# Kernel optimization log

Hardware: AMD Instinct MI355X
Metric: run time of the kernel (lower is better)

Reference implementation:

```python
import jax, jax.numpy as jnp
import numpy as np

DIM = 1024
HEADS = 16
DIM_HEAD = 64
INNER = HEADS * DIM_HEAD
SCALE = 8.0  # default scale in plain_cosine_sim_attention
EPS = 1e-5


def setup_inputs() -> dict:
    key = jax.random.key(0)
    ks = jax.random.split(key, 5)
    b, n = 2, 2048
    x = jax.random.normal(ks[0], (b, n, DIM), dtype=jnp.float32)
    ln_w = jnp.ones((DIM,), dtype=jnp.float32)
    ln_b = jnp.zeros((DIM,), dtype=jnp.float32)
    W_qkv = jax.random.normal(ks[1], (DIM, 3 * INNER), dtype=jnp.float32) * (DIM ** -0.5)
    W_out = jax.random.normal(ks[2], (INNER, DIM), dtype=jnp.float32) * (INNER ** -0.5)
    return {"x": x, "ln_w": ln_w, "ln_b": ln_b, "W_qkv": W_qkv, "W_out": W_out}


def _l2norm(t):
    return t / jnp.clip(jnp.linalg.norm(t, axis=-1, keepdims=True), 1e-12)


def reference(x, ln_w, ln_b, W_qkv, W_out):
    b, n, _ = x.shape
    # LayerNorm
    mu = jnp.mean(x, axis=-1, keepdims=True)
    var = jnp.var(x, axis=-1, keepdims=True)
    xn = (x - mu) * jax.lax.rsqrt(var + EPS) * ln_w + ln_b
    # QKV projection (no bias)
    qkv = xn @ W_qkv  # [b, n, 3*inner]
    q, k, v = jnp.split(qkv, 3, axis=-1)
    # [b, n, h*d] -> [b, h, n, d]
    def to_heads(t):
        return t.reshape(b, n, HEADS, DIM_HEAD).transpose(0, 2, 1, 3)
    q, k, v = to_heads(q), to_heads(k), to_heads(v)
    # cosine-sim attention: l2-normalize q, k then scaled dot product
    q = _l2norm(q)
    k = _l2norm(k)
    sim = jnp.einsum('bhid,bhjd->bhij', q, k) * SCALE
    # causal mask
    causal = jnp.tril(jnp.ones((n, n), dtype=bool))
    sim = jnp.where(causal, sim, jnp.finfo(sim.dtype).min)
    attn = jax.nn.softmax(sim, axis=-1)
    o = jnp.einsum('bhij,bhjd->bhid', attn, v)
    # [b, h, n, d] -> [b, n, h*d]
    o = o.transpose(0, 2, 1, 3).reshape(b, n, INNER)
    return o @ W_out
```

## Files before the change

kernel.cpp:

```cpp
#include <hip/hip_runtime.h>
#include <hip/hip_bf16.h>

typedef __attribute__((ext_vector_type(8))) short short8;
typedef __attribute__((ext_vector_type(4))) float floatx4;

__device__ __forceinline__ ushort f2bf(float f) {
    union { __hip_bfloat16 h; ushort u; } cv;
    cv.h = __float2bfloat16(f);
    return cv.u;
}
__device__ __forceinline__ float bf2f(ushort u) {
    union { ushort u; __hip_bfloat16 h; } cv;
    cv.u = u;
    return __bfloat162float(cv.h);
}
__device__ __forceinline__ ushort f2bf_rtz(float f) {
    union { float f; unsigned u; } cv;
    cv.f = f;
    return (ushort)(cv.u >> 16);
}

typedef __attribute__((address_space(1))) void* gas1_t;
typedef __attribute__((address_space(3))) void* las3_t;
__device__ __forceinline__ void cp16(const ushort* g, ushort* l) {
    __builtin_amdgcn_global_load_lds((gas1_t)(unsigned long long)g,
                                     (las3_t)(unsigned long long)l, 16, 0, 0);
}

__global__ __launch_bounds__(256) void prep_w_ln(const float* __restrict__ Wqkv,
                                                 const float* __restrict__ Wout,
                                                 ushort* __restrict__ WqkvT,
                                                 ushort* __restrict__ WoutT,
                                                 const float* __restrict__ x,
                                                 const float* __restrict__ lw,
                                                 const float* __restrict__ lb,
                                                 ushort* __restrict__ xn) {
    const int id = blockIdx.x;
    const int tid = threadIdx.x;
    if (id < 4096) {
        __shared__ float tile[32][33];
        int bx = id & 127, by = id >> 7;
        const float* in; ushort* out; int R = 1024, C;
        if (bx < 96) { in = Wqkv; out = WqkvT; C = 3072; }
        else { in = Wout; out = WoutT; C = 1024; bx -= 96; }
        int c0 = bx * 32, r0 = by * 32;
        int tx = tid & 31, ty = tid >> 5;
        for (int j = 0; j < 32; j += 8)
            tile[ty + j][tx] = in[(size_t)(r0 + ty + j) * C + c0 + tx];
        __syncthreads();
        for (int j = 0; j < 32; j += 8)
            out[(size_t)(c0 + ty + j) * R + r0 + tx] = f2bf(tile[tx][ty + j]);
    } else {
        int row = id - 4096;
        const float4* xr = (const float4*)(x + (size_t)row * 1024);
        float4 v = xr[tid];
        float s = v.x + v.y + v.z + v.w;
        float sq = v.x * v.x + v.y * v.y + v.z * v.z + v.w * v.w;
        for (int off = 32; off; off >>= 1) {
            s += __shfl_xor(s, off);
            sq += __shfl_xor(sq, off);
        }
        __shared__ float ls[4], lq[4];
        int wave = tid >> 6, lane = tid & 63;
        if (lane == 0) { ls[wave] = s; lq[wave] = sq; }
        __syncthreads();
        s = ls[0] + ls[1] + ls[2] + ls[3];
        sq = lq[0] + lq[1] + lq[2] + lq[3];
        float mu = s * (1.0f / 1024.0f);
        float var = sq * (1.0f / 1024.0f) - mu * mu;
        float rs = rsqrtf(var + 1e-5f);
        const float4* wr = (const float4*)lw;
        const float4* br = (const float4*)lb;
        float4 wv = wr[tid], bv = br[tid];
        ushort4 o;
        o.x = f2bf((v.x - mu) * rs * wv.x + bv.x);
        o.y = f2bf((v.y - mu) * rs * wv.y + bv.y);
        o.z = f2bf((v.z - mu) * rs * wv.z + bv.z);
        o.w = f2bf((v.w - mu) * rs * wv.w + bv.w);
        *(ushort4*)&xn[(size_t)row * 1024 + tid * 4] = o;
    }
}

__global__ __launch_bounds__(256) void gemm_qkv_fused(const ushort* __restrict__ A,
                                                      const ushort* __restrict__ Bt,
                                                      ushort* __restrict__ Qt,
                                                      ushort* __restrict__ Kt,
                                                      ushort* __restrict__ Vb) {
    __shared__ ushort smem[18432];
    const int K = 1024, T = 32;
    const int id = blockIdx.x;
    const int xcd = id & 7, r_ = id >> 3;
    const int bm = (xcd * 4 + r_ / 24) * 128;
    const int bn = r_ % 24;
    const int tid = threadIdx.x;
    const int wave = tid >> 6, lane = tid & 63;
    const int quad = lane >> 4, l15 = lane & 15;
    const int wm = (wave >> 1) * 64, wn = (wave & 1) * 64;

    const int s0 = tid, s1 = tid + 256;
    const int row0 = s0 >> 2, src0 = (s0 & 3) ^ (row0 & 3);
    const int row1 = s1 >> 2, src1 = (s1 & 3) ^ (row1 & 3);

    floatx4 acc[4][4];
    floatx4 z4 = {0.f, 0.f, 0.f, 0.f};
    for (int mi = 0; mi < 4; mi++)
        for (int ni = 0; ni < 4; ni++) acc[mi][ni] = z4;

    const ushort* Ap0 = A + (size_t)(bm + row0) * K + src0 * 8;
    const ushort* Ap1 = A + (size_t)(bm + row1) * K + src1 * 8;
    const ushort* Bp0 = Bt + (size_t)(bn * 128 + row0) * K + src0 * 8;
    const ushort* Bp1 = Bt + (size_t)(bn * 128 + row1) * K + src1 * 8;

    ushort* As = smem;
    ushort* Bs = smem + 8192;

    cp16(Ap0, &As[wave * 512]);
    cp16(Ap1, &As[2048 + wave * 512]);
    cp16(Bp0, &Bs[wave * 512]);
    cp16(Bp1, &Bs[2048 + wave * 512]);

    for (int t = 0; t < T; t++) {
        __syncthreads();
        if (t + 1 < T) {
            const int nb = (t + 1) & 1;
            const int k0n = (t + 1) << 5;
            cp16(Ap0 + k0n, &As[nb * 4096 + wave * 512]);
            cp16(Ap1 + k0n, &As[nb * 4096 + 2048 + wave * 512]);
            cp16(Bp0 + k0n, &Bs[nb * 4096 + wave * 512]);
            cp16(Bp1 + k0n, &Bs[nb * 4096 + 2048 + wave * 512]);
        }
        const ushort* Ab = As + (t & 1) * 4096;
        const ushort* Bb = Bs + (t & 1) * 4096;
        short8 af[4], bfr[4];
        for (int mi = 0; mi < 4; mi++) {
            int ra = wm + mi * 16 + l15;
            af[mi] = *(const short8*)&Ab[ra * 32 + ((quad ^ (ra & 3)) << 3)];
        }
        for (int ni = 0; ni < 4; ni++) {
            int rb = wn + ni * 16 + l15;
            bfr[ni] = *(const short8*)&Bb[rb * 32 + ((quad ^ (rb & 3)) << 3)];
        }
        for (int mi = 0; mi < 4; mi++)
            for (int ni = 0; ni < 4; ni++)
                acc[mi][ni] = __builtin_amdgcn_mfma_f32_16x16x32_bf16(
                    af[mi], bfr[ni], acc[mi][ni], 0, 0, 0);
    }

    const int col_base = bn * 128 + wn;
    const int type = col_base >> 10;
    const int h = (col_base & 1023) >> 6;
    const int row_base = bm + wm;

    if (type < 2) {
        ushort* dst = (type == 0) ? Qt : Kt;
        for (int mi = 0; mi < 4; mi++) {
            for (int r = 0; r < 4; r++) {
                float ss = 0.f;
                for (int ni = 0; ni < 4; ni++) ss += acc[mi][ni][r] * acc[mi][ni][r];
                for (int off = 1; off < 16; off <<= 1) ss += __shfl_xor(ss, off);
                float inv = rsqrtf(fmaxf(ss, 1e-24f));
                int rg = row_base + mi * 16 + quad * 4 + r;
                int bb = rg >> 11, n = rg & 2047;
                size_t orow = ((size_t)(bb * 16 + h) * 2048 + n) * 64;
                for (int ni = 0; ni < 4; ni++)
                    dst[orow + ni * 16 + l15] = f2bf(acc[mi][ni][r] * inv);
            }
        }
    } else {
        __syncthreads();
        ushort* tr = smem + wave * 4608;
        for (int mi = 0; mi < 4; mi++)
            for (int ni = 0; ni < 4; ni++)
                for (int r = 0; r < 4; r++) {
                    int row_l = mi * 16 + quad * 4 + r;
                    int col_l = ni * 16 + l15;
                    tr[col_l * 72 + row_l] = f2bf(acc[mi][ni][r]);
                }
        int bb = row_base >> 11, n0 = row_base & 2047;
        size_t vbase = ((size_t)(bb * 16 + h) * 32 + (n0 >> 6)) * 4096;
        const int dl = lane >> 3, nc = (lane & 7) * 8;
        for (int i = 0; i < 8; i++) {
            int d = dl + i * 8;
            short8 val = *(const short8*)&tr[d * 72 + nc];
            *(short8*)&Vb[vbase + (size_t)d * 64 + nc] = val;
        }
    }
}

__global__ __launch_bounds__(256) void gemm_out(const ushort* __restrict__ A,
                                                const ushort* __restrict__ Bt,
                                                float* __restrict__ C) {
    __shared__ ushort As[2][64 * 32];
    __shared__ ushort Bs[2][64 * 32];
    const int K = 1024, N = 1024;
    const int id = blockIdx.x;
    const int xcd = id & 7, r_ = id >> 3;
    const int bm = (xcd * 8 + (r_ >> 4)) * 64;
    const int bn = (r_ & 15) * 64;
    const int tid = threadIdx.x;
    const int wave = tid >> 6, lane = tid & 63;
    const int quad = lane >> 4, l15 = lane & 15;
    const int wm = (wave >> 1) * 32, wn = (wave & 1) * 32;

    const int row0 = tid >> 2, src0 = (tid & 3) ^ (row0 & 3);

    floatx4 acc[2][2];
    floatx4 z4 = {0.f, 0.f, 0.f, 0.f};
    for (int mi = 0; mi < 2; mi++)
        for (int ni = 0; ni < 2; ni++) acc[mi][ni] = z4;

    const ushort* Ap0 = A + (size_t)(bm + row0) * K + src0 * 8;
    const ushort* Bp0 = Bt + (size_t)(bn + row0) * K + src0 * 8;

    const int T = K >> 5;
    cp16(Ap0, &As[0][wave * 512]);
    cp16(Bp0, &Bs[0][wave * 512]);

    for (int t = 0; t < T; t++) {
        __syncthreads();
        if (t + 1 < T) {
            const int nb = (t + 1) & 1;
            const int k0n = (t + 1) << 5;
            cp16(Ap0 + k0n, &As[nb][wave * 512]);
            cp16(Bp0 + k0n, &Bs[nb][wave * 512]);
        }
        const ushort* Ab = As[t & 1];
        const ushort* Bb = Bs[t & 1];
        short8 af[2], bfr[2];
        for (int mi = 0; mi < 2; mi++) {
            int ra = wm + mi * 16 + l15;
            af[mi] = *(const short8*)&Ab[ra * 32 + ((quad ^ (ra & 3)) << 3)];
        }
        for (int ni = 0; ni < 2; ni++) {
            int rb = wn + ni * 16 + l15;
            bfr[ni] = *(const short8*)&Bb[rb * 32 + ((quad ^ (rb & 3)) << 3)];
        }
        for (int mi = 0; mi < 2; mi++)
            for (int ni = 0; ni < 2; ni++)
                acc[mi][ni] = __builtin_amdgcn_mfma_f32_16x16x32_bf16(
                    af[mi], bfr[ni], acc[mi][ni], 0, 0, 0);
    }
    for (int mi = 0; mi < 2; mi++)
        for (int ni = 0; ni < 2; ni++)
            for (int r = 0; r < 4; r++) {
                int row = bm + wm + mi * 16 + quad * 4 + r;
                int col = bn + wn + ni * 16 + l15;
                C[(size_t)row * N + col] = acc[mi][ni][r];
            }
}

#define LOG2E8 11.541560327111707f

__global__ __launch_bounds__(256) void flash_attn(const ushort* __restrict__ Qt,
                                                  const ushort* __restrict__ Kt,
                                                  const ushort* __restrict__ Vb,
                                                  ushort* __restrict__ O) {
    const int id = blockIdx.x;
    const int xcd = id & 7, r_ = id >> 3;
    const int bh = xcd * 4 + (r_ >> 4);
    const int pairi = r_ & 15;
    const int b = bh >> 4, h = bh & 15;
    const int tid = threadIdx.x;
    const int wave = tid >> 6, lane = tid & 63;
    const int quad = lane >> 4, l15 = lane & 15;

    __shared__ ushort Ks[2][64 * 64];
    __shared__ ushort Vs[2][64 * 64];
    __shared__ ushort Ps[4][16 * 64];

    const int ch0 = tid, ch1 = tid + 256;
    const int r0 = ch0 >> 3, sg0 = (ch0 & 7) ^ (r0 & 7);
    const int r1 = ch1 >> 3, sg1 = (ch1 & 7) ^ (r1 & 7);

    const ushort* Kp0 = Kt + ((size_t)bh * 2048 + r0) * 64 + sg0 * 8;
    const ushort* Kp1 = Kt + ((size_t)bh * 2048 + r1) * 64 + sg1 * 8;
    const ushort* Vp0 = Vb + (size_t)bh * 131072 + r0 * 64 + sg0 * 8;
    const ushort* Vp1 = Vb + (size_t)bh * 131072 + r1 * 64 + sg1 * 8;

    floatx4 z4 = {0.f, 0.f, 0.f, 0.f};

    for (int pass = 0; pass < 2; pass++) {
        const int qt = pass ? (31 - pairi) : pairi;
        const int q0 = qt * 64;

        const ushort* Qp = Qt + ((size_t)bh * 2048 + q0 + wave * 16 + l15) * 64;
        short8 qf0 = *(const short8*)(Qp + quad * 8);
        short8 qf1 = *(const short8*)(Qp + 32 + quad * 8);

        float rs_acc[4] = {0.f, 0.f, 0.f, 0.f};
        floatx4 o_acc[4];
        for (int ni = 0; ni < 4; ni++) o_acc[ni] = z4;

        __syncthreads();
        cp16(Kp0, &Ks[0][wave * 512]);
        cp16(Kp1, &Ks[0][2048 + wave * 512]);
        cp16(Vp0, &Vs[0][wave * 512]);
        cp16(Vp1, &Vs[0][2048 + wave * 512]);

        for (int kt = 0; kt <= qt; kt++) {
            __syncthreads();
            if (kt < qt) {
                const int nb2 = (kt + 1) & 1;
                const size_t to = (size_t)(kt + 1) * 4096;
                cp16(Kp0 + to, &Ks[nb2][wave * 512]);
                cp16(Kp1 + to, &Ks[nb2][2048 + wave * 512]);
                cp16(Vp0 + to, &Vs[nb2][wave * 512]);
                cp16(Vp1 + to, &Vs[nb2][2048 + wave * 512]);
            }
            const ushort* Kb = Ks[kt & 1];
            const ushort* Vb_ = Vs[kt & 1];

            floatx4 s_acc[4];
            for (int ni = 0; ni < 4; ni++) s_acc[ni] = z4;
            for (int ni = 0; ni < 4; ni++) {
                int rb = ni * 16 + l15;
                short8 kf0 = *(const short8*)&Kb[rb * 64 + ((quad ^ (rb & 7)) << 3)];
                short8 kf1 = *(const short8*)&Kb[rb * 64 + (((quad + 4) ^ (rb & 7)) << 3)];
                s_acc[ni] = __builtin_amdgcn_mfma_f32_16x16x32_bf16(qf0, kf0, s_acc[ni], 0, 0, 0);
                s_acc[ni] = __builtin_amdgcn_mfma_f32_16x16x32_bf16(qf1, kf1, s_acc[ni], 0, 0, 0);
            }

            const bool diag = (kt == qt);
            for (int ni = 0; ni < 4; ni++) {
                const int col_loc = ni * 16 + l15;
                const int chnk = col_loc >> 3;
                for (int r = 0; r < 4; r++) {
                    const int row_l = quad * 4 + r;
                    float e = __builtin_amdgcn_exp2f(
                        fmaf(s_acc[ni][r], LOG2E8, -LOG2E8));
                    if (diag && col_loc > wave * 16 + row_l) e = 0.f;
                    rs_acc[r] += e;
                    Ps[wave][row_l * 64 + (((chnk ^ (row_l & 7)) << 3) | (col_loc & 7))] =
                        f2bf_rtz(e);
                }
            }

            short8 pa0 = *(const short8*)&Ps[wave][l15 * 64 + ((quad ^ (l15 & 7)) << 3)];
            short8 pa1 = *(const short8*)&Ps[wave][l15 * 64 + (((quad + 4) ^ (l15 & 7)) << 3)];
            for (int ni = 0; ni < 4; ni++) {
                int rv = ni * 16 + l15;
                short8 v0 = *(const short8*)&Vb_[rv * 64 + ((quad ^ (rv & 7)) << 3)];
                short8 v1 = *(const short8*)&Vb_[rv * 64 + (((quad + 4) ^ (rv & 7)) << 3)];
                o_acc[ni] = __builtin_amdgcn_mfma_f32_16x16x32_bf16(pa0, v0, o_acc[ni], 0, 0, 0);
                o_acc[ni] = __builtin_amdgcn_mfma_f32_16x16x32_bf16(pa1, v1, o_acc[ni], 0, 0, 0);
            }
        }

        for (int r = 0; r < 4; r++) {
            float rs = rs_acc[r];
            for (int off = 1; off < 16; off <<= 1) rs += __shfl_xor(rs, off);
            float inv = 1.0f / rs;
            int grow = q0 + wave * 16 + quad * 4 + r;
            size_t rowbase = ((size_t)b * 2048 + grow) * 1024 + h * 64;
            for (int ni = 0; ni < 4; ni++)
                O[rowbase + ni * 16 + l15] = f2bf(o_acc[ni][r] * inv);
        }
    }
}

extern "C" void kernel_launch(void* const* d_in, const int* in_sizes, int n_in,
                              void* d_out, int out_size, void* d_ws, size_t ws_size,
                              hipStream_t stream) {
    const float* x = (const float*)d_in[0];
    const float* ln_w = (const float*)d_in[1];
    const float* ln_b = (const float*)d_in[2];
    const float* W_qkv = (const float*)d_in[3];
    const float* W_out = (const float*)d_in[4];

    char* w = (char*)d_ws;
    ushort* xn    = (ushort*)(w);
    ushort* obuf  = (ushort*)(w);
    ushort* WqkvT = (ushort*)(w + (8ull << 20));
    ushort* WoutT = (ushort*)(w + (14ull << 20));
    ushort* Vb    = (ushort*)(w + (16ull << 20));
    ushort* Qt    = (ushort*)(w + (24ull << 20));
    ushort* Kt    = (ushort*)(w + (32ull << 20));

    prep_w_ln<<<8192, 256, 0, stream>>>(W_qkv, W_out, WqkvT, WoutT, x, ln_w, ln_b, xn);
    gemm_qkv_fused<<<768, 256, 0, stream>>>(xn, WqkvT, Qt, Kt, Vb);
    flash_attn<<<512, 256, 0, stream>>>(Qt, Kt, Vb, obuf);
    gemm_out<<<1024, 256, 0, stream>>>(obuf, WoutT, (float*)d_out);
}
```

Before: 175.8 us.

## Split flash attention into one block per query tile and deepen gemm_out K-step

```diff
diff --git a/kernel.cpp b/kernel.cpp
--- a/kernel.cpp
+++ b/kernel.cpp
@@ -190,8 +190,8 @@
 __global__ __launch_bounds__(256) void gemm_out(const ushort* __restrict__ A,
                                                 const ushort* __restrict__ Bt,
                                                 float* __restrict__ C) {
-    __shared__ ushort As[2][64 * 32];
-    __shared__ ushort Bs[2][64 * 32];
+    __shared__ ushort As[2][4096];
+    __shared__ ushort Bs[2][4096];
     const int K = 1024, N = 1024;
     const int id = blockIdx.x;
     const int xcd = id & 7, r_ = id >> 3;
@@ -202,43 +202,56 @@
     const int quad = lane >> 4, l15 = lane & 15;
     const int wm = (wave >> 1) * 32, wn = (wave & 1) * 32;
 
-    const int row0 = tid >> 2, src0 = (tid & 3) ^ (row0 & 3);
+    const int ch0 = tid, ch1 = tid + 256;
+    const int r0 = ch0 >> 3, sg0 = (ch0 & 7) ^ (r0 & 7);
+    const int r1 = ch1 >> 3, sg1 = (ch1 & 7) ^ (r1 & 7);
 
     floatx4 acc[2][2];
     floatx4 z4 = {0.f, 0.f, 0.f, 0.f};
     for (int mi = 0; mi < 2; mi++)
         for (int ni = 0; ni < 2; ni++) acc[mi][ni] = z4;
 
-    const ushort* Ap0 = A + (size_t)(bm + row0) * K + src0 * 8;
-    const ushort* Bp0 = Bt + (size_t)(bn + row0) * K + src0 * 8;
-
-    const int T = K >> 5;
+    const ushort* Ap0 = A + (size_t)(bm + r0) * K + sg0 * 8;
+    const ushort* Ap1 = A + (size_t)(bm + r1) * K + sg1 * 8;
+    const ushort* Bp0 = Bt + (size_t)(bn + r0) * K + sg0 * 8;
+    const ushort* Bp1 = Bt + (size_t)(bn + r1) * K + sg1 * 8;
+
+    const int T = 16;
     cp16(Ap0, &As[0][wave * 512]);
+    cp16(Ap1, &As[0][2048 + wave * 512]);
     cp16(Bp0, &Bs[0][wave * 512]);
+    cp16(Bp1, &Bs[0][2048 + wave * 512]);
 
     for (int t = 0; t < T; t++) {
         __syncthreads();
         if (t + 1 < T) {
             const int nb = (t + 1) & 1;
-            const int k0n = (t + 1) << 5;
+            const int k0n = (t + 1) << 6;
             cp16(Ap0 + k0n, &As[nb][wave * 512]);
+            cp16(Ap1 + k0n, &As[nb][2048 + wave * 512]);
             cp16(Bp0 + k0n, &Bs[nb][wave * 512]);
+            cp16(Bp1 + k0n, &Bs[nb][2048 + wave * 512]);
         }
         const ushort* Ab = As[t & 1];
         const ushort* Bb = Bs[t & 1];
-        short8 af[2], bfr[2];
+        short8 a0[2], a1[2], b0[2], b1[2];
         for (int mi = 0; mi < 2; mi++) {
             int ra = wm + mi * 16 + l15;
-            af[mi] = *(const short8*)&Ab[ra * 32 + ((quad ^ (ra & 3)) << 3)];
+            a0[mi] = *(const short8*)&Ab[ra * 64 + ((quad ^ (ra & 7)) << 3)];
+            a1[mi] = *(const short8*)&Ab[ra * 64 + (((quad + 4) ^ (ra & 7)) << 3)];
         }
         for (int ni = 0; ni < 2; ni++) {
             int rb = wn + ni * 16 + l15;
-            bfr[ni] = *(const short8*)&Bb[rb * 32 + ((quad ^ (rb & 3)) << 3)];
+            b0[ni] = *(const short8*)&Bb[rb * 64 + ((quad ^ (rb & 7)) << 3)];
+            b1[ni] = *(const short8*)&Bb[rb * 64 + (((quad + 4) ^ (rb & 7)) << 3)];
         }
         for (int mi = 0; mi < 2; mi++)
-            for (int ni = 0; ni < 2; ni++)
+            for (int ni = 0; ni < 2; ni++) {
                 acc[mi][ni] = __builtin_amdgcn_mfma_f32_16x16x32_bf16(
-                    af[mi], bfr[ni], acc[mi][ni], 0, 0, 0);
+                    a0[mi], b0[ni], acc[mi][ni], 0, 0, 0);
+                acc[mi][ni] = __builtin_amdgcn_mfma_f32_16x16x32_bf16(
+                    a1[mi], b1[ni], acc[mi][ni], 0, 0, 0);
+            }
     }
     for (int mi = 0; mi < 2; mi++)
         for (int ni = 0; ni < 2; ni++)
@@ -257,8 +270,11 @@
                                                   ushort* __restrict__ O) {
     const int id = blockIdx.x;
     const int xcd = id & 7, r_ = id >> 3;
-    const int bh = xcd * 4 + (r_ >> 4);
-    const int pairi = r_ & 15;
+    const int bh = xcd + ((r_ & 3) << 3);
+    const int u = r_ >> 2;
+    const int s_ = u >> 3, g = u & 7;
+    const int qt = (s_ == 0) ? g : (s_ == 1) ? (15 - g)
+                 : (s_ == 2) ? (16 + g) : (31 - g);
     const int b = bh >> 4, h = bh & 15;
     const int tid = threadIdx.x;
     const int wave = tid >> 6, lane = tid & 63;
@@ -279,82 +295,77 @@
 
     floatx4 z4 = {0.f, 0.f, 0.f, 0.f};
 
-    for (int pass = 0; pass < 2; pass++) {
-        const int qt = pass ? (31 - pairi) : pairi;
-        const int q0 = qt * 64;
-
-        const ushort* Qp = Qt + ((size_t)bh * 2048 + q0 + wave * 16 + l15) * 64;
-        short8 qf0 = *(const short8*)(Qp + quad * 8);
-        short8 qf1 = *(const short8*)(Qp + 32 + quad * 8);
-
-        float rs_acc[4] = {0.f, 0.f, 0.f, 0.f};
-        floatx4 o_acc[4];
-        for (int ni = 0; ni < 4; ni++) o_acc[ni] = z4;
-
-        __syncthreads();
-        cp16(Kp0, &Ks[0][wave * 512]);
-        cp16(Kp1, &Ks[0][2048 + wave * 512]);
-        cp16(Vp0, &Vs[0][wave * 512]);
-        cp16(Vp1, &Vs[0][2048 + wave * 512]);
-
-        for (int kt = 0; kt <= qt; kt++) {
-            __syncthreads();
-            if (kt < qt) {
-                const int nb2 = (kt + 1) & 1;
-                const size_t to = (size_t)(kt + 1) * 4096;
-                cp16(Kp0 + to, &Ks[nb2][wave * 512]);
-                cp16(Kp1 + to, &Ks[nb2][2048 + wave * 512]);
-                cp16(Vp0 + to, &Vs[nb2][wave * 512]);
-                cp16(Vp1 + to, &Vs[nb2][2048 + wave * 512]);
+    const int q0 = qt * 64;
+    const ushort* Qp = Qt + ((size_t)bh * 2048 + q0 + wave * 16 + l15) * 64;
+    short8 qf0 = *(const short8*)(Qp + quad * 8);
+    short8 qf1 = *(const short8*)(Qp + 32 + quad * 8);
+
+    float rs_acc[4] = {0.f, 0.f, 0.f, 0.f};
+    floatx4 o_acc[4];
+    for (int ni = 0; ni < 4; ni++) o_acc[ni] = z4;
+
+    cp16(Kp0, &Ks[0][wave * 512]);
+    cp16(Kp1, &Ks[0][2048 + wave * 512]);
+    cp16(Vp0, &Vs[0][wave * 512]);
+    cp16(Vp1, &Vs[0][2048 + wave * 512]);
+
+    for (int kt = 0; kt <= qt; kt++) {
+        __syncthreads();
+        if (kt < qt) {
+            const int nb2 = (kt + 1) & 1;
+            const size_t to = (size_t)(kt + 1) * 4096;
+            cp16(Kp0 + to, &Ks[nb2][wave * 512]);
+            cp16(Kp1 + to, &Ks[nb2][2048 + wave * 512]);
+            cp16(Vp0 + to, &Vs[nb2][wave * 512]);
+            cp16(Vp1 + to, &Vs[nb2][2048 + wave * 512]);
+        }
+        const ushort* Kb = Ks[kt & 1];
+        const ushort* Vb_ = Vs[kt & 1];
+
+        floatx4 s_acc[4];
+        for (int ni = 0; ni < 4; ni++) s_acc[ni] = z4;
+        for (int ni = 0; ni < 4; ni++) {
+            int rb = ni * 16 + l15;
+            short8 kf0 = *(const short8*)&Kb[rb * 64 + ((quad ^ (rb & 7)) << 3)];
+            short8 kf1 = *(const short8*)&Kb[rb * 64 + (((quad + 4) ^ (rb & 7)) << 3)];
+            s_acc[ni] = __builtin_amdgcn_mfma_f32_16x16x32_bf16(qf0, kf0, s_acc[ni], 0, 0, 0);
+            s_acc[ni] = __builtin_amdgcn_mfma_f32_16x16x32_bf16(qf1, kf1, s_acc[ni], 0, 0, 0);
+        }
+
+        const bool diag = (kt == qt);
+        for (int ni = 0; ni < 4; ni++) {
+            const int col_loc = ni * 16 + l15;
+            const int chnk = col_loc >> 3;
+            for (int r = 0; r < 4; r++) {
+                const int row_l = quad * 4 + r;
+                float e = __builtin_amdgcn_exp2f(
+                    fmaf(s_acc[ni][r], LOG2E8, -LOG2E8));
+                if (diag && col_loc > wave * 16 + row_l) e = 0.f;
+                rs_acc[r] += e;
+                Ps[wave][row_l * 64 + (((chnk ^ (row_l & 7)) << 3) | (col_loc & 7))] =
+                    f2bf_rtz(e);
             }
-            const ushort* Kb = Ks[kt & 1];
-            const ushort* Vb_ = Vs[kt & 1];
-
-            floatx4 s_acc[4];
-            for (int ni = 0; ni < 4; ni++) s_acc[ni] = z4;
-            for (int ni = 0; ni < 4; ni++) {
-                int rb = ni * 16 + l15;
-                short8 kf0 = *(const short8*)&Kb[rb * 64 + ((quad ^ (rb & 7)) << 3)];
-                short8 kf1 = *(const short8*)&Kb[rb * 64 + (((quad + 4) ^ (rb & 7)) << 3)];
-                s_acc[ni] = __builtin_amdgcn_mfma_f32_16x16x32_bf16(qf0, kf0, s_acc[ni], 0, 0, 0);
-                s_acc[ni] = __builtin_amdgcn_mfma_f32_16x16x32_bf16(qf1, kf1, s_acc[ni], 0, 0, 0);
-            }
-
-            const bool diag = (kt == qt);
-            for (int ni = 0; ni < 4; ni++) {
-                const int col_loc = ni * 16 + l15;
-                const int chnk = col_loc >> 3;
-                for (int r = 0; r < 4; r++) {
-                    const int row_l = quad * 4 + r;
-                    float e = __builtin_amdgcn_exp2f(
-                        fmaf(s_acc[ni][r], LOG2E8, -LOG2E8));
-                    if (diag && col_loc > wave * 16 + row_l) e = 0.f;
-                    rs_acc[r] += e;
-                    Ps[wave][row_l * 64 + (((chnk ^ (row_l & 7)) << 3) | (col_loc & 7))] =
-                        f2bf_rtz(e);
-                }
-            }
-
-            short8 pa0 = *(const short8*)&Ps[wave][l15 * 64 + ((quad ^ (l15 & 7)) << 3)];
-            short8 pa1 = *(const short8*)&Ps[wave][l15 * 64 + (((quad + 4) ^ (l15 & 7)) << 3)];
-            for (int ni = 0; ni < 4; ni++) {
-                int rv = ni * 16 + l15;
-                short8 v0 = *(const short8*)&Vb_[rv * 64 + ((quad ^ (rv & 7)) << 3)];
-                short8 v1 = *(const short8*)&Vb_[rv * 64 + (((quad + 4) ^ (rv & 7)) << 3)];
-                o_acc[ni] = __builtin_amdgcn_mfma_f32_16x16x32_bf16(pa0, v0, o_acc[ni], 0, 0, 0);
-                o_acc[ni] = __builtin_amdgcn_mfma_f32_16x16x32_bf16(pa1, v1, o_acc[ni], 0, 0, 0);
-            }
-        }
-
-        for (int r = 0; r < 4; r++) {
-            float rs = rs_acc[r];
-            for (int off = 1; off < 16; off <<= 1) rs += __shfl_xor(rs, off);
-            float inv = 1.0f / rs;
-            int grow = q0 + wave * 16 + quad * 4 + r;
-            size_t rowbase = ((size_t)b * 2048 + grow) * 1024 + h * 64;
-            for (int ni = 0; ni < 4; ni++)
-                O[rowbase + ni * 16 + l15] = f2bf(o_acc[ni][r] * inv);
-        }
+        }
+
+        short8 pa0 = *(const short8*)&Ps[wave][l15 * 64 + ((quad ^ (l15 & 7)) << 3)];
+        short8 pa1 = *(const short8*)&Ps[wave][l15 * 64 + (((quad + 4) ^ (l15 & 7)) << 3)];
+        for (int ni = 0; ni < 4; ni++) {
+            int rv = ni * 16 + l15;
+            short8 v0 = *(const short8*)&Vb_[rv * 64 + ((quad ^ (rv & 7)) << 3)];
+            short8 v1 = *(const short8*)&Vb_[rv * 64 + (((quad + 4) ^ (rv & 7)) << 3)];
+            o_acc[ni] = __builtin_amdgcn_mfma_f32_16x16x32_bf16(pa0, v0, o_acc[ni], 0, 0, 0);
+            o_acc[ni] = __builtin_amdgcn_mfma_f32_16x16x32_bf16(pa1, v1, o_acc[ni], 0, 0, 0);
+        }
+    }
+
+    for (int r = 0; r < 4; r++) {
+        float rs = rs_acc[r];
+        for (int off = 1; off < 16; off <<= 1) rs += __shfl_xor(rs, off);
+        float inv = 1.0f / rs;
+        int grow = q0 + wave * 16 + quad * 4 + r;
+        size_t rowbase = ((size_t)b * 2048 + grow) * 1024 + h * 64;
+        for (int ni = 0; ni < 4; ni++)
+            O[rowbase + ni * 16 + l15] = f2bf(o_acc[ni][r] * inv);
     }
 }
 
@@ -378,6 +389,6 @@
 
     prep_w_ln<<<8192, 256, 0, stream>>>(W_qkv, W_out, WqkvT, WoutT, x, ln_w, ln_b, xn);
     gemm_qkv_fused<<<768, 256, 0, stream>>>(xn, WqkvT, Qt, Kt, Vb);
-    flash_attn<<<512, 256, 0, stream>>>(Qt, Kt, Vb, obuf);
+    flash_attn<<<1024, 256, 0, stream>>>(Qt, Kt, Vb, obuf);
     gemm_out<<<1024, 256, 0, stream>>>(obuf, WoutT, (float*)d_out);
 }
```

Measured after the change: 173.0 us. Within noise of the previous version (-1.6%).
